# Kernel tuning notes

Hardware: AMD Instinct MI355X
Metric: run time of the kernel (lower is better)

Reference implementation:

```python
import jax, jax.numpy as jnp
import numpy as np

NUM_CAPSULE = 32
DIM_CAPSULE = 16
ROUTINGS = 3
EPS = 1e-7  # K.epsilon()


def squash(x, axis=-1):
    s2 = jnp.sum(jnp.square(x), axis=axis, keepdims=True) + EPS
    scale = jnp.sqrt(s2) / (0.5 + s2)
    return scale * x


def setup_inputs() -> dict:
    key = jax.random.key(0)
    kx, kw = jax.random.split(key)
    x = jax.random.normal(kx, (128, 2048, 128), dtype=jnp.float32)
    # glorot-uniform-scale init for (in_dim, num_capsule*dim_capsule)
    fan_in, fan_out = 128, NUM_CAPSULE * DIM_CAPSULE
    limit = np.sqrt(6.0 / (fan_in + fan_out)).astype(np.float32)
    kernel = jax.random.uniform(kw, (fan_in, fan_out), dtype=jnp.float32,
                                minval=-limit, maxval=limit)
    return {"x": x, "kernel": kernel}


def reference(x, kernel):
    B, N, _ = x.shape
    # share_weights=True: 1x1 conv1d == matmul over input_dim_capsule
    hat = jnp.einsum('bnd,dm->bnm', x, kernel)            # (B, N, C*D)
    hat = hat.reshape(B, N, NUM_CAPSULE, DIM_CAPSULE)
    hat = jnp.transpose(hat, (0, 2, 1, 3))                # (B, C, N, D)
    b = jnp.zeros(hat.shape[:3], dtype=hat.dtype)         # (B, C, N)
    o = None
    for i in range(ROUTINGS):
        c = jax.nn.softmax(b, axis=1)                     # softmax over output capsules
        o = squash(jnp.einsum('bcn,bcnd->bcd', c, hat))   # (B, C, D)
        if i < ROUTINGS - 1:
            b = jnp.einsum('bcd,bcnd->bcn', o, hat)       # agreement (replaces b, per code)
    return o
```

## Files before the change

kernel.cpp:

```cpp
#include <hip/hip_runtime.h>
#include <hip/hip_bf16.h>


#define BATCH 128
#define SEQ   2048
#define KDIM  128
#define NCAP  32
#define DCAP  16

typedef __attribute__((ext_vector_type(8))) short bf16x8;
typedef __attribute__((ext_vector_type(4))) float f32x4;

__device__ __forceinline__ short f2bf(float f) {
  unsigned u = __float_as_uint(f);
  u = u + 0x7fffu + ((u >> 16) & 1u);
  return (short)(u >> 16);
}

__global__ void colsum_k(const float* __restrict__ x, float* __restrict__ S) {
  int b  = blockIdx.x >> 3;
  int ch = blockIdx.x & 7;
  int t  = threadIdx.x;
  int k = t & 127, rh = t >> 7;
  const float* xp = x + ((size_t)b * SEQ + ch * 256 + rh) * KDIM + k;
  float acc = 0.f;
  #pragma unroll 8
  for (int r = 0; r < 256; r += 2) acc += xp[(size_t)r * KDIM];
  __shared__ float red[256];
  red[t] = acc;
  __syncthreads();
  if (t < 128) atomicAdd(&S[b * KDIM + k], red[t] + red[t + 128]);
}

__global__ void route_small_k(const float* __restrict__ W,
                              const float* __restrict__ S,
                              const float* __restrict__ y,
                              short* __restrict__ wt,
                              float* __restrict__ out,
                              int mode) {
  int b = blockIdx.x;
  int t = threadIdx.x;
  int c = t >> 4, d = t & 15;
  float s = 0.f;
  if (mode == 0) {
    const float* Sp = S + b * KDIM;
    #pragma unroll 4
    for (int k = 0; k < KDIM; ++k) s += Sp[k] * W[k * 512 + c * DCAP + d];
    s *= (1.f / 32.f);
  } else {
    const float* yp = y + ((size_t)b * NCAP + c) * KDIM;
    #pragma unroll 4
    for (int k = 0; k < KDIM; ++k) s += yp[k] * W[k * 512 + c * DCAP + d];
  }
  float s2 = s * s;
  s2 += __shfl_xor(s2, 1);
  s2 += __shfl_xor(s2, 2);
  s2 += __shfl_xor(s2, 4);
  s2 += __shfl_xor(s2, 8);
  s2 += 1e-7f;
  float scale = sqrtf(s2) / (0.5f + s2);
  float o = scale * s;
  if (mode == 2) { out[(size_t)b * 512 + t] = o; return; }
  __shared__ float olds[512];
  olds[t] = o;
  __syncthreads();
  int kb = t & 15;
  #pragma unroll
  for (int i = 0; i < 8; ++i) {
    int k = kb + i * 16;
    float acc = 0.f;
    #pragma unroll
    for (int dd = 0; dd < DCAP; ++dd)
      acc += olds[c * DCAP + dd] * W[k * 512 + c * DCAP + dd];
    wt[((size_t)b * NCAP + c) * KDIM + k] = f2bf(acc);
  }
}

__global__ __launch_bounds__(256, 2) void pass_k(const float* __restrict__ x,
                                                 const short* __restrict__ wt,
                                                 float* __restrict__ yout) {
  __shared__ char lx[32768];
  __shared__ char lw[8192];
  __shared__ char lcn[8192];
  __shared__ float yred[4096];

  int b = blockIdx.x >> 2, pb = blockIdx.x & 3;
  int t = threadIdx.x;
  int wv = t >> 6, lane = t & 63, l15 = lane & 15, lg = lane >> 4;

  {
    int e = t * 16, c = e >> 7, k = e & 127;
    const short* gw = wt + (size_t)b * 4096 + e;
    bf16x8 w0 = *(const bf16x8*)gw;
    bf16x8 w1 = *(const bf16x8*)(gw + 8);
    int swz = (c & 7) << 4;
    *(bf16x8*)(lw + ((c * 256 + k * 2) ^ swz)) = w0;
    *(bf16x8*)(lw + ((c * 256 + (k + 8) * 2) ^ swz)) = w1;
  }

  f32x4 zz = {0.f, 0.f, 0.f, 0.f};
  f32x4 yacc[2][8];
  #pragma unroll
  for (int i = 0; i < 2; ++i)
    #pragma unroll
    for (int j = 0; j < 8; ++j) yacc[i][j] = zz;

  const size_t xbase = ((size_t)b * SEQ + (size_t)pb * 512) * KDIM;

  for (int chunk = 0; chunk < 4; ++chunk) {
    {
      int oct = t & 15, rsub = t >> 4;
      #pragma unroll
      for (int sub = 0; sub < 8; ++sub) {
        int r = sub * 16 + rsub;
        const float* gp = x + xbase + (size_t)(chunk * 128 + r) * KDIM + oct * 8;
        float4 f0 = *(const float4*)gp;
        float4 f1 = *(const float4*)(gp + 4);
        bf16x8 v;
        short* vp = (short*)&v;
        vp[0] = f2bf(f0.x); vp[1] = f2bf(f0.y); vp[2] = f2bf(f0.z); vp[3] = f2bf(f0.w);
        vp[4] = f2bf(f1.x); vp[5] = f2bf(f1.y); vp[6] = f2bf(f1.z); vp[7] = f2bf(f1.w);
        *(bf16x8*)(lx + ((r * 256 + oct * 16) ^ ((r & 7) << 4))) = v;
      }
    }
    __syncthreads();

    f32x4 sc[2][2];
    sc[0][0] = zz; sc[0][1] = zz; sc[1][0] = zz; sc[1][1] = zz;
    #pragma unroll
    for (int ks = 0; ks < 4; ++ks) {
      bf16x8 a[2], bw[2];
      #pragma unroll
      for (int mi = 0; mi < 2; ++mi) {
        int row = wv * 32 + mi * 16 + l15;
        a[mi] = *(const bf16x8*)(lx + ((row * 256 + ks * 64 + lg * 16) ^ ((row & 7) << 4)));
      }
      #pragma unroll
      for (int ct = 0; ct < 2; ++ct) {
        int cc = ct * 16 + l15;
        bw[ct] = *(const bf16x8*)(lw + ((cc * 256 + ks * 64 + lg * 16) ^ ((cc & 7) << 4)));
      }
      #pragma unroll
      for (int mi = 0; mi < 2; ++mi)
        #pragma unroll
        for (int ct = 0; ct < 2; ++ct)
          sc[mi][ct] = __builtin_amdgcn_mfma_f32_16x16x32_bf16(a[mi], bw[ct], sc[mi][ct], 0, 0, 0);
    }

    #pragma unroll
    for (int mi = 0; mi < 2; ++mi) {
      #pragma unroll
      for (int r = 0; r < 4; ++r) {
        float v0 = sc[mi][0][r], v1 = sc[mi][1][r];
        float mx = fmaxf(v0, v1);
        mx = fmaxf(mx, __shfl_xor(mx, 1));
        mx = fmaxf(mx, __shfl_xor(mx, 2));
        mx = fmaxf(mx, __shfl_xor(mx, 4));
        mx = fmaxf(mx, __shfl_xor(mx, 8));
        float e0 = __expf(v0 - mx), e1 = __expf(v1 - mx);
        float sm = e0 + e1;
        sm += __shfl_xor(sm, 1);
        sm += __shfl_xor(sm, 2);
        sm += __shfl_xor(sm, 4);
        sm += __shfl_xor(sm, 8);
        float inv = 1.f / sm;
        int row = wv * 32 + mi * 16 + lg * 4 + r;
        int c0 = l15, c1 = 16 + l15;
        *(short*)(lcn + ((c0 * 256 + row * 2) ^ ((c0 & 7) << 4))) = f2bf(e0 * inv);
        *(short*)(lcn + ((c1 * 256 + row * 2) ^ ((c1 & 7) << 4))) = f2bf(e1 * inv);
      }
    }
    __syncthreads();

    {
      bf16x8 a2[2];
      #pragma unroll
      for (int m2 = 0; m2 < 2; ++m2) {
        int cc = m2 * 16 + l15;
        a2[m2] = *(const bf16x8*)(lcn + ((cc * 256 + wv * 64 + lg * 16) ^ ((cc & 7) << 4)));
      }
      #pragma unroll
      for (int nt = 0; nt < 8; ++nt) {
        bf16x8 bx;
        short* bp = (short*)&bx;
        int col = nt * 16 + l15;
        int rbase = wv * 32 + lg * 8;
        #pragma unroll
        for (int j = 0; j < 8; ++j) {
          int row = rbase + j;
          bp[j] = *(const short*)(lx + ((row * 256 + col * 2) ^ ((row & 7) << 4)));
        }
        yacc[0][nt] = __builtin_amdgcn_mfma_f32_16x16x32_bf16(a2[0], bx, yacc[0][nt], 0, 0, 0);
        yacc[1][nt] = __builtin_amdgcn_mfma_f32_16x16x32_bf16(a2[1], bx, yacc[1][nt], 0, 0, 0);
      }
    }
    __syncthreads();
  }

  #pragma unroll 1
  for (int round = 0; round < 4; ++round) {
    if (wv == round) {
      #pragma unroll
      for (int m2 = 0; m2 < 2; ++m2)
        #pragma unroll
        for (int nt = 0; nt < 8; ++nt)
          #pragma unroll
          for (int r = 0; r < 4; ++r) {
            int cc = m2 * 16 + lg * 4 + r;
            int kk = nt * 16 + l15;
            if (round == 0) yred[cc * 128 + kk]  = yacc[m2][nt][r];
            else            yred[cc * 128 + kk] += yacc[m2][nt][r];
          }
    }
    __syncthreads();
  }
  #pragma unroll
  for (int i = 0; i < 16; ++i)
    atomicAdd(&yout[(size_t)b * 4096 + i * 256 + t], yred[i * 256 + t]);
}

extern "C" void kernel_launch(void* const* d_in, const int* in_sizes, int n_in,
                              void* d_out, int out_size, void* d_ws, size_t ws_size,
                              hipStream_t stream) {
  const float* x = (const float*)d_in[0];
  const float* W = (const float*)d_in[1];
  float* out = (float*)d_out;
  char* ws = (char*)d_ws;
  float* S  = (float*)ws;
  float* y1 = (float*)(ws + 65536);
  float* y2 = (float*)(ws + 65536 + 2097152);
  short* wt = (short*)(ws + 65536 + 2 * 2097152);

  hipMemsetAsync(d_ws, 0, 65536 + 2 * 2097152, stream);

  colsum_k<<<dim3(1024), dim3(256), 0, stream>>>(x, S);
  route_small_k<<<dim3(128), dim3(512), 0, stream>>>(W, S, nullptr, wt, nullptr, 0);
  pass_k<<<dim3(512), dim3(256), 0, stream>>>(x, wt, y1);
  route_small_k<<<dim3(128), dim3(512), 0, stream>>>(W, nullptr, y1, wt, nullptr, 1);
  pass_k<<<dim3(512), dim3(256), 0, stream>>>(x, wt, y2);
  route_small_k<<<dim3(128), dim3(512), 0, stream>>>(W, nullptr, y2, nullptr, out, 2);
}
```

Baseline: 344.5 us.

## Pre-convert x to swizzled bf16 once, drop atomics and reshape small kernels

```diff
diff --git a/kernel.cpp b/kernel.cpp
--- a/kernel.cpp
+++ b/kernel.cpp
@@ -2,11 +2,8 @@
 #include <hip/hip_bf16.h>
 
 
-#define BATCH 128
-#define SEQ   2048
-#define KDIM  128
-#define NCAP  32
-#define DCAP  16
+#define SEQ 2048
+#define KD  128
 
 typedef __attribute__((ext_vector_type(8))) short bf16x8;
 typedef __attribute__((ext_vector_type(4))) float f32x4;
@@ -16,75 +13,97 @@
   u = u + 0x7fffu + ((u >> 16) & 1u);
   return (short)(u >> 16);
 }
-
-__global__ void colsum_k(const float* __restrict__ x, float* __restrict__ S) {
-  int b  = blockIdx.x >> 3;
-  int ch = blockIdx.x & 7;
-  int t  = threadIdx.x;
-  int k = t & 127, rh = t >> 7;
-  const float* xp = x + ((size_t)b * SEQ + ch * 256 + rh) * KDIM + k;
-  float acc = 0.f;
-  #pragma unroll 8
-  for (int r = 0; r < 256; r += 2) acc += xp[(size_t)r * KDIM];
-  __shared__ float red[256];
-  red[t] = acc;
+__device__ __forceinline__ int swz(int row) {
+  return ((row & 7) << 4) ^ ((row & 24) << 2);
+}
+
+__global__ __launch_bounds__(256) void prep_k(const float* __restrict__ x,
+                                              short* __restrict__ xs,
+                                              float* __restrict__ S) {
+  int blk = blockIdx.x;
+  int t = threadIdx.x, oct = t & 15, rsub = t >> 4;
+  size_t row0 = (size_t)blk * 128;
+  char* dst = (char*)xs + (size_t)blk * 32768;
+  float sac[8] = {0.f,0.f,0.f,0.f,0.f,0.f,0.f,0.f};
+  #pragma unroll
+  for (int sub = 0; sub < 8; ++sub) {
+    int r = sub * 16 + rsub;
+    const float* gp = x + (row0 + r) * KD + oct * 8;
+    float4 f0 = *(const float4*)gp, f1 = *(const float4*)(gp + 4);
+    bf16x8 v; short* vp = (short*)&v;
+    vp[0] = f2bf(f0.x); vp[1] = f2bf(f0.y); vp[2] = f2bf(f0.z); vp[3] = f2bf(f0.w);
+    vp[4] = f2bf(f1.x); vp[5] = f2bf(f1.y); vp[6] = f2bf(f1.z); vp[7] = f2bf(f1.w);
+    sac[0] += f0.x; sac[1] += f0.y; sac[2] += f0.z; sac[3] += f0.w;
+    sac[4] += f1.x; sac[5] += f1.y; sac[6] += f1.z; sac[7] += f1.w;
+    *(bf16x8*)(dst + ((r * 256 + oct * 16) ^ swz(r))) = v;
+  }
+  __shared__ float red[2048];
+  float4* rp = (float4*)&red[rsub * 128 + oct * 8];
+  rp[0] = make_float4(sac[0], sac[1], sac[2], sac[3]);
+  rp[1] = make_float4(sac[4], sac[5], sac[6], sac[7]);
   __syncthreads();
-  if (t < 128) atomicAdd(&S[b * KDIM + k], red[t] + red[t + 128]);
-}
-
-__global__ void route_small_k(const float* __restrict__ W,
-                              const float* __restrict__ S,
-                              const float* __restrict__ y,
-                              short* __restrict__ wt,
-                              float* __restrict__ out,
-                              int mode) {
-  int b = blockIdx.x;
-  int t = threadIdx.x;
-  int c = t >> 4, d = t & 15;
+  if (t < 128) {
+    float s = 0.f;
+    #pragma unroll
+    for (int i = 0; i < 16; ++i) s += red[i * 128 + t];
+    atomicAdd(&S[(blk >> 4) * KD + t], s);
+  }
+}
+
+__global__ __launch_bounds__(64) void small_k(const float* __restrict__ W,
+                                              const float* __restrict__ S,
+                                              const float* __restrict__ yp,
+                                              short* __restrict__ wt,
+                                              float* __restrict__ out,
+                                              int mode) {
+  int b = blockIdx.x >> 5, c = blockIdx.x & 31;
+  int l = threadIdx.x, d = l & 15, kg = l >> 4;
+  const float* Wc = W + c * 16;
   float s = 0.f;
   if (mode == 0) {
-    const float* Sp = S + b * KDIM;
-    #pragma unroll 4
-    for (int k = 0; k < KDIM; ++k) s += Sp[k] * W[k * 512 + c * DCAP + d];
+    const float* Sp = S + b * KD;
+    #pragma unroll 8
+    for (int i = 0; i < 32; ++i) { int k = kg * 32 + i; s += Sp[k] * Wc[k * 512 + d]; }
     s *= (1.f / 32.f);
   } else {
-    const float* yp = y + ((size_t)b * NCAP + c) * KDIM;
-    #pragma unroll 4
-    for (int k = 0; k < KDIM; ++k) s += yp[k] * W[k * 512 + c * DCAP + d];
-  }
+    const float* y0 = yp + (size_t)b * 4 * 4096 + c * KD;
+    #pragma unroll 8
+    for (int i = 0; i < 32; ++i) {
+      int k = kg * 32 + i;
+      float yv = y0[k] + y0[4096 + k] + y0[8192 + k] + y0[12288 + k];
+      s += yv * Wc[k * 512 + d];
+    }
+  }
+  s += __shfl_xor(s, 16); s += __shfl_xor(s, 32);
   float s2 = s * s;
-  s2 += __shfl_xor(s2, 1);
-  s2 += __shfl_xor(s2, 2);
-  s2 += __shfl_xor(s2, 4);
-  s2 += __shfl_xor(s2, 8);
+  s2 += __shfl_xor(s2, 1); s2 += __shfl_xor(s2, 2);
+  s2 += __shfl_xor(s2, 4); s2 += __shfl_xor(s2, 8);
   s2 += 1e-7f;
-  float scale = sqrtf(s2) / (0.5f + s2);
-  float o = scale * s;
-  if (mode == 2) { out[(size_t)b * 512 + t] = o; return; }
-  __shared__ float olds[512];
-  olds[t] = o;
+  float o = (sqrtf(s2) / (0.5f + s2)) * s;
+  if (mode == 2) { if (l < 16) out[(size_t)b * 512 + c * 16 + l] = o; return; }
+  __shared__ float olds[16];
+  if (l < 16) olds[l] = o;
   __syncthreads();
-  int kb = t & 15;
-  #pragma unroll
-  for (int i = 0; i < 8; ++i) {
-    int k = kb + i * 16;
+  #pragma unroll
+  for (int h = 0; h < 2; ++h) {
+    int k = l + h * 64;
     float acc = 0.f;
     #pragma unroll
-    for (int dd = 0; dd < DCAP; ++dd)
-      acc += olds[c * DCAP + dd] * W[k * 512 + c * DCAP + dd];
-    wt[((size_t)b * NCAP + c) * KDIM + k] = f2bf(acc);
-  }
-}
-
-__global__ __launch_bounds__(256, 2) void pass_k(const float* __restrict__ x,
+    for (int dd = 0; dd < 16; ++dd) acc += olds[dd] * Wc[k * 512 + dd];
+    wt[((size_t)b * 32 + c) * KD + k] = f2bf(acc);
+  }
+}
+
+__global__ __launch_bounds__(256, 2) void pass_k(const short* __restrict__ xs,
                                                  const short* __restrict__ wt,
                                                  float* __restrict__ yout) {
-  __shared__ char lx[32768];
-  __shared__ char lw[8192];
-  __shared__ char lcn[8192];
-  __shared__ float yred[4096];
-
-  int b = blockIdx.x >> 2, pb = blockIdx.x & 3;
+  __shared__ char ldsbuf[49152];
+  char* lx  = ldsbuf;
+  char* lw  = ldsbuf + 32768;
+  char* lcn = ldsbuf + 40960;
+  float* yred = (float*)ldsbuf;
+
+  int b = blockIdx.x >> 2;
   int t = threadIdx.x;
   int wv = t >> 6, lane = t & 63, l15 = lane & 15, lg = lane >> 4;
 
@@ -93,9 +112,9 @@
     const short* gw = wt + (size_t)b * 4096 + e;
     bf16x8 w0 = *(const bf16x8*)gw;
     bf16x8 w1 = *(const bf16x8*)(gw + 8);
-    int swz = (c & 7) << 4;
-    *(bf16x8*)(lw + ((c * 256 + k * 2) ^ swz)) = w0;
-    *(bf16x8*)(lw + ((c * 256 + (k + 8) * 2) ^ swz)) = w1;
+    int sw = (c & 7) << 4;
+    *(bf16x8*)(lw + ((c * 256 + k * 2) ^ sw)) = w0;
+    *(bf16x8*)(lw + ((c * 256 + (k + 8) * 2) ^ sw)) = w1;
   }
 
   f32x4 zz = {0.f, 0.f, 0.f, 0.f};
@@ -105,22 +124,13 @@
     #pragma unroll
     for (int j = 0; j < 8; ++j) yacc[i][j] = zz;
 
-  const size_t xbase = ((size_t)b * SEQ + (size_t)pb * 512) * KDIM;
-
   for (int chunk = 0; chunk < 4; ++chunk) {
     {
-      int oct = t & 15, rsub = t >> 4;
+      const char* gs = (const char*)xs + ((size_t)blockIdx.x * 4 + chunk) * 32768;
       #pragma unroll
       for (int sub = 0; sub < 8; ++sub) {
-        int r = sub * 16 + rsub;
-        const float* gp = x + xbase + (size_t)(chunk * 128 + r) * KDIM + oct * 8;
-        float4 f0 = *(const float4*)gp;
-        float4 f1 = *(const float4*)(gp + 4);
-        bf16x8 v;
-        short* vp = (short*)&v;
-        vp[0] = f2bf(f0.x); vp[1] = f2bf(f0.y); vp[2] = f2bf(f0.z); vp[3] = f2bf(f0.w);
-        vp[4] = f2bf(f1.x); vp[5] = f2bf(f1.y); vp[6] = f2bf(f1.z); vp[7] = f2bf(f1.w);
-        *(bf16x8*)(lx + ((r * 256 + oct * 16) ^ ((r & 7) << 4))) = v;
+        int off = sub * 4096 + t * 16;
+        *(bf16x8*)(lx + off) = *(const bf16x8*)(gs + off);
       }
     }
     __syncthreads();
@@ -133,7 +143,7 @@
       #pragma unroll
       for (int mi = 0; mi < 2; ++mi) {
         int row = wv * 32 + mi * 16 + l15;
-        a[mi] = *(const bf16x8*)(lx + ((row * 256 + ks * 64 + lg * 16) ^ ((row & 7) << 4)));
+        a[mi] = *(const bf16x8*)(lx + ((row * 256 + ks * 64 + lg * 16) ^ swz(row)));
       }
       #pragma unroll
       for (int ct = 0; ct < 2; ++ct) {
@@ -159,10 +169,8 @@
         mx = fmaxf(mx, __shfl_xor(mx, 8));
         float e0 = __expf(v0 - mx), e1 = __expf(v1 - mx);
         float sm = e0 + e1;
-        sm += __shfl_xor(sm, 1);
-        sm += __shfl_xor(sm, 2);
-        sm += __shfl_xor(sm, 4);
-        sm += __shfl_xor(sm, 8);
+        sm += __shfl_xor(sm, 1); sm += __shfl_xor(sm, 2);
+        sm += __shfl_xor(sm, 4); sm += __shfl_xor(sm, 8);
         float inv = 1.f / sm;
         int row = wv * 32 + mi * 16 + lg * 4 + r;
         int c0 = l15, c1 = 16 + l15;
@@ -188,7 +196,7 @@
         #pragma unroll
         for (int j = 0; j < 8; ++j) {
           int row = rbase + j;
-          bp[j] = *(const short*)(lx + ((row * 256 + col * 2) ^ ((row & 7) << 4)));
+          bp[j] = *(const short*)(lx + ((row * 256 + col * 2) ^ swz(row)));
         }
         yacc[0][nt] = __builtin_amdgcn_mfma_f32_16x16x32_bf16(a2[0], bx, yacc[0][nt], 0, 0, 0);
         yacc[1][nt] = __builtin_amdgcn_mfma_f32_16x16x32_bf16(a2[1], bx, yacc[1][nt], 0, 0, 0);
@@ -214,9 +222,9 @@
     }
     __syncthreads();
   }
-  #pragma unroll
-  for (int i = 0; i < 16; ++i)
-    atomicAdd(&yout[(size_t)b * 4096 + i * 256 + t], yred[i * 256 + t]);
+  float* yo = yout + (size_t)blockIdx.x * 4096;
+  #pragma unroll
+  for (int i = 0; i < 16; ++i) yo[i * 256 + t] = yred[i * 256 + t];
 }
 
 extern "C" void kernel_launch(void* const* d_in, const int* in_sizes, int n_in,
@@ -228,15 +236,16 @@
   char* ws = (char*)d_ws;
   float* S  = (float*)ws;
   float* y1 = (float*)(ws + 65536);
-  float* y2 = (float*)(ws + 65536 + 2097152);
-  short* wt = (short*)(ws + 65536 + 2 * 2097152);
-
-  hipMemsetAsync(d_ws, 0, 65536 + 2 * 2097152, stream);
-
-  colsum_k<<<dim3(1024), dim3(256), 0, stream>>>(x, S);
-  route_small_k<<<dim3(128), dim3(512), 0, stream>>>(W, S, nullptr, wt, nullptr, 0);
-  pass_k<<<dim3(512), dim3(256), 0, stream>>>(x, wt, y1);
-  route_small_k<<<dim3(128), dim3(512), 0, stream>>>(W, nullptr, y1, wt, nullptr, 1);
-  pass_k<<<dim3(512), dim3(256), 0, stream>>>(x, wt, y2);
-  route_small_k<<<dim3(128), dim3(512), 0, stream>>>(W, nullptr, y2, nullptr, out, 2);
-}
+  float* y2 = (float*)(ws + 65536 + 8388608);
+  short* wt = (short*)(ws + 65536 + 16777216);
+  short* xs = (short*)(ws + 20971520);
+
+  hipMemsetAsync(S, 0, 65536, stream);
+
+  prep_k <<<dim3(2048), dim3(256), 0, stream>>>(x, xs, S);
+  small_k<<<dim3(4096), dim3(64), 0, stream>>>(W, S, nullptr, wt, nullptr, 0);
+  pass_k <<<dim3(512), dim3(256), 0, stream>>>(xs, wt, y1);
+  small_k<<<dim3(4096), dim3(64), 0, stream>>>(W, nullptr, y1, wt, nullptr, 1);
+  pass_k <<<dim3(512), dim3(256), 0, stream>>>(xs, wt, y2);
+  small_k<<<dim3(4096), dim3(64), 0, stream>>>(W, nullptr, y2, nullptr, out, 2);
+}
```

Result: faster. 299.6 us (-13.0%).
